# Performance work log

Hardware: AMD Instinct MI355X
Metric: run time of the kernel (lower is better)

Reference implementation:

```python
import jax, jax.numpy as jnp
import numpy as np

L, D, H, M, NC = 12, 768, 12, 3072, 1000
P, IMG, C = 16, 224, 3
HD = D // H // 2  # 32: diff-attn head dim (2*H query heads of HD, H value heads of 2*HD)
B = 32
N = (IMG // P) ** 2 + 1  # 197
EPS = 1e-5


def _layernorm(x, s, b):
    mu = x.mean(-1, keepdims=True)
    var = ((x - mu) ** 2).mean(-1, keepdims=True)
    return (x - mu) * jax.lax.rsqrt(var + EPS) * s + b


def _rmsnorm(x, s):
    ms = (x * x).mean(-1, keepdims=True)
    return x * jax.lax.rsqrt(ms + EPS) * s


def _diff_attn(x, qw, kw, vw, ow, lq1, lk1, lq2, lk2, sls, lam_init):
    b, n, _ = x.shape
    q = (x @ qw).reshape(b, n, 2 * H, HD)
    k = (x @ kw).reshape(b, n, 2 * H, HD)
    v = (x @ vw).reshape(b, n, H, 2 * HD)
    scores = jnp.einsum('bnhd,bmhd->bhnm', q, k) * (HD ** -0.5)
    attn = jax.nn.softmax(scores, axis=-1)  # [b, 2H, n, n]
    lam = jnp.exp(jnp.sum(lq1 * lk1)) - jnp.exp(jnp.sum(lq2 * lk2)) + lam_init
    attn = attn.reshape(b, H, 2, n, n)
    attn = attn[:, :, 0] - lam * attn[:, :, 1]  # differential attention map
    out = jnp.einsum('bhnm,bmhd->bnhd', attn, v)  # [b, n, H, 2*HD]
    out = _rmsnorm(out, sls) * (1.0 - lam_init)
    return out.reshape(b, n, D) @ ow


def _forward(x, conv_w, conv_b, cls_token, pos_emb,
             ln1_s, ln1_b, q_w, k_w, v_w, o_w, lq1, lk1, lq2, lk2, subln_s,
             ln2_s, ln2_b, w1, b1, w2, b2, lnf_s, lnf_b, head_w, head_b):
    # patch embed: conv stride=patch, then flatten to tokens
    h = jax.lax.conv_general_dilated(x, conv_w, (P, P), 'VALID',
                                     dimension_numbers=('NCHW', 'OIHW', 'NCHW'))
    h = h + conv_b[None, :, None, None]
    bsz = x.shape[0]
    h = h.reshape(bsz, D, -1).transpose(0, 2, 1)  # [B, 196, D]
    h = jnp.concatenate([jnp.broadcast_to(cls_token, (bsz, 1, D)), h], axis=1)
    h = h + pos_emb
    for i in range(L):
        lam_init = 0.8 - 0.6 * np.exp(-0.3 * i)
        a = _diff_attn(_layernorm(h, ln1_s[i], ln1_b[i]), q_w[i], k_w[i], v_w[i], o_w[i],
                       lq1[i], lk1[i], lq2[i], lk2[i], subln_s[i], lam_init)
        h = h + a
        m = _layernorm(h, ln2_s[i], ln2_b[i])
        m = jax.nn.gelu(m @ w1[i] + b1[i]) @ w2[i] + b2[i]
        h = h + m
    h = _layernorm(h, lnf_s, lnf_b)
    return h[:, 0] @ head_w + head_b


def setup_inputs() -> dict:
    key = jax.random.key(0)
    ks = iter(jax.random.split(key, 40))
    def rn(shape, s=0.02):
        return jax.random.normal(next(ks), shape, jnp.float32) * s
    return {
        'x': jax.random.normal(next(ks), (B, C, IMG, IMG), jnp.float32),
        'conv_w': rn((D, C, P, P)), 'conv_b': jnp.zeros((D,), jnp.float32),
        'cls_token': jnp.zeros((1, 1, D), jnp.float32),
        'pos_emb': rn((1, N, D)),
        'ln1_s': jnp.ones((L, D), jnp.float32), 'ln1_b': jnp.zeros((L, D), jnp.float32),
        'q_w': rn((L, D, D)), 'k_w': rn((L, D, D)), 'v_w': rn((L, D, D)), 'o_w': rn((L, D, D)),
        'lq1': rn((L, HD), 0.1), 'lk1': rn((L, HD), 0.1),
        'lq2': rn((L, HD), 0.1), 'lk2': rn((L, HD), 0.1),
        'subln_s': jnp.ones((L, 2 * HD), jnp.float32),
        'ln2_s': jnp.ones((L, D), jnp.float32), 'ln2_b': jnp.zeros((L, D), jnp.float32),
        'w1': rn((L, D, M)), 'b1': jnp.zeros((L, M), jnp.float32),
        'w2': rn((L, M, D)), 'b2': jnp.zeros((L, D), jnp.float32),
        'lnf_s': jnp.ones((D,), jnp.float32), 'lnf_b': jnp.zeros((D,), jnp.float32),
        'head_w': rn((D, NC)), 'head_b': jnp.zeros((NC,), jnp.float32),
    }


def reference(x, conv_w, conv_b, cls_token, pos_emb,
              ln1_s, ln1_b, q_w, k_w, v_w, o_w, lq1, lk1, lq2, lk2, subln_s,
              ln2_s, ln2_b, w1, b1, w2, b2, lnf_s, lnf_b, head_w, head_b):
    return _forward(x, conv_w, conv_b, cls_token, pos_emb,
                    ln1_s, ln1_b, q_w, k_w, v_w, o_w, lq1, lk1, lq2, lk2, subln_s,
                    ln2_s, ln2_b, w1, b1, w2, b2, lnf_s, lnf_b, head_w, head_b)
```

## Files before the change

kernel.cpp:

```cpp
#include <hip/hip_runtime.h>
#include <cmath>


typedef unsigned short u16;
typedef u16 u16x4 __attribute__((ext_vector_type(4)));
typedef u16 u16x8 __attribute__((ext_vector_type(8)));
typedef float fx4 __attribute__((ext_vector_type(4)));
typedef __bf16 bf16x8 __attribute__((ext_vector_type(8)));

#define MROWS 6304
#define MPAD  6400

__device__ __forceinline__ float bf2f(u16 u) {
  union { unsigned int i; float f; } c; c.i = ((unsigned int)u) << 16; return c.f;
}
__device__ __forceinline__ u16 f2bf(float f) {
  union { float f; unsigned int i; } c; c.f = f;
  return (u16)((c.i + 0x7FFFu + ((c.i >> 16) & 1u)) >> 16);
}
__device__ __forceinline__ float gelu_f(float x) {
  float u = 0.7978845608028654f * (x + 0.044715f * x * x * x);
  u = fminf(fmaxf(u, -30.f), 30.f);
  float e = __expf(2.f * u);
  return 0.5f * x * (1.f + (e - 1.f) / (e + 1.f));
}

__device__ __forceinline__ void gload16(const void* g, void* l) {
  __builtin_amdgcn_global_load_lds(
      (const __attribute__((address_space(1))) void*)g,
      (__attribute__((address_space(3))) void*)l, 16, 0, 0);
}

__device__ __forceinline__ int xcd_swz(int orig, int nwg) {
  int q = nwg >> 3, r = nwg & 7;
  int x = orig & 7, i = orig >> 3;
  return (x < r ? x * (q + 1) : r * (q + 1) + (x - r) * q) + i;
}

enum { EP_F32 = 0, EP_BF16 = 1, EP_GELU_BF16 = 2, EP_RESID_F32 = 3 };

template<int MODE>
__device__ __forceinline__ void ep_store(void* outp, const float* __restrict__ resid,
                                         size_t m, size_t n, size_t N, float v) {
  if (MODE == EP_GELU_BF16)      ((u16*)outp)[m * N + n] = f2bf(gelu_f(v));
  else if (MODE == EP_BF16)      ((u16*)outp)[m * N + n] = f2bf(v);
  else if (MODE == EP_RESID_F32) ((float*)outp)[m * N + n] = resid[m * N + n] + v;
  else                           ((float*)outp)[m * N + n] = v;
}

template<int MODE, bool BIAS>
__device__ __forceinline__
void gemm_big_body(const u16* __restrict__ A, const u16* __restrict__ Bt,
                   const float* __restrict__ bias, const float* __restrict__ resid,
                   void* __restrict__ outp, int M, int N, int K, int GX)
{
  __shared__ unsigned char lds[2][2 * 128 * 64 * 2];
  const int tid = threadIdx.x;
  const int lane = tid & 63, w = tid >> 6;
  const int g = lane >> 4, l = lane & 15;
  const int wr = w >> 1, wc = w & 1;
  const int wg = xcd_swz(blockIdx.x, gridDim.x);
  const int bm = (wg % GX) * 128, bn = (wg / GX) * 128;

  const int swz_half = ((lane & 7) ^ ((lane >> 3) & 7)) << 3;
  const int srow = 32 * w + (lane >> 3);
  const u16* gA = A + (size_t)(bm + srow) * K + swz_half;
  const u16* gB = Bt + (size_t)(bn + srow) * K + swz_half;

  fx4 acc[4][4] = {};

  auto STAGE = [&](int buf, int kt) {
    unsigned char* bA = &lds[buf][0] + 4096 * w;
    unsigned char* bB = bA + 16384;
    #pragma unroll
    for (int c = 0; c < 4; ++c) {
      gload16(gA + (size_t)(8 * c) * K + kt, bA + (8 * c) * 128);
      gload16(gB + (size_t)(8 * c) * K + kt, bB + (8 * c) * 128);
    }
  };

  STAGE(0, 0);
  __syncthreads();
  int cur = 0;
  for (int kt = 0; kt < K; kt += 64) {
    if (kt + 64 < K) STAGE(cur ^ 1, kt + 64);
    const unsigned char* As = &lds[cur][0];
    const unsigned char* Bs = As + 16384;
    #pragma unroll
    for (int kk = 0; kk < 2; ++kk) {
      bf16x8 af[4], bfr[4];
      #pragma unroll
      for (int i = 0; i < 4; ++i) {
        int ar = wr * 64 + i * 16 + l;
        af[i] = *(const bf16x8*)(As + ar * 128 + ((kk * 64 + g * 16) ^ ((ar & 7) << 4)));
        int br = wc * 64 + i * 16 + l;
        bfr[i] = *(const bf16x8*)(Bs + br * 128 + ((kk * 64 + g * 16) ^ ((br & 7) << 4)));
      }
      #pragma unroll
      for (int i = 0; i < 4; ++i)
        #pragma unroll
        for (int j = 0; j < 4; ++j)
          acc[i][j] = __builtin_amdgcn_mfma_f32_16x16x32_bf16(af[i], bfr[j], acc[i][j], 0, 0, 0);
    }
    __syncthreads();
    cur ^= 1;
  }
  #pragma unroll
  for (int j = 0; j < 4; ++j) {
    int n = bn + wc * 64 + j * 16 + l;
    float bv = BIAS ? bias[n] : 0.f;
    #pragma unroll
    for (int i = 0; i < 4; ++i) {
      int mbase = bm + wr * 64 + i * 16 + g * 4;
      #pragma unroll
      for (int q = 0; q < 4; ++q) {
        int m = mbase + q;
        if (m < M) ep_store<MODE>(outp, resid, m, n, N, acc[i][j][q] + bv);
      }
    }
  }
}

template<int MODE, bool BIAS>
__device__ __forceinline__
void gemm_n64_body(const u16* __restrict__ A, const u16* __restrict__ Bt,
                   const float* __restrict__ bias, const float* __restrict__ resid,
                   void* __restrict__ outp, int M, int N, int K, int NT)
{
  __shared__ unsigned char lds[2][(128 + 64) * 64 * 2];
  const int tid = threadIdx.x;
  const int lane = tid & 63, w = tid >> 6;
  const int g = lane >> 4, l = lane & 15;
  const int wg = xcd_swz(blockIdx.x, gridDim.x);
  const int bm = (wg / NT) * 128, bn = (wg % NT) * 64;

  const int swz_half = ((lane & 7) ^ ((lane >> 3) & 7)) << 3;
  const u16* gA = A + (size_t)(bm + 32 * w + (lane >> 3)) * K + swz_half;
  const u16* gB = Bt + (size_t)(bn + 16 * w + (lane >> 3)) * K + swz_half;

  fx4 acc[2][4] = {};

  auto STAGE = [&](int buf, int kt) {
    unsigned char* bA = &lds[buf][0] + 4096 * w;
    unsigned char* bB = &lds[buf][0] + 16384 + 2048 * w;
    #pragma unroll
    for (int c = 0; c < 4; ++c)
      gload16(gA + (size_t)(8 * c) * K + kt, bA + (8 * c) * 128);
    #pragma unroll
    for (int c = 0; c < 2; ++c)
      gload16(gB + (size_t)(8 * c) * K + kt, bB + (8 * c) * 128);
  };

  STAGE(0, 0);
  __syncthreads();
  int cur = 0;
  for (int kt = 0; kt < K; kt += 64) {
    if (kt + 64 < K) STAGE(cur ^ 1, kt + 64);
    const unsigned char* As = &lds[cur][0];
    const unsigned char* Bs = As + 16384;
    #pragma unroll
    for (int kk = 0; kk < 2; ++kk) {
      bf16x8 af[2], bfr[4];
      #pragma unroll
      for (int i = 0; i < 2; ++i) {
        int ar = w * 32 + i * 16 + l;
        af[i] = *(const bf16x8*)(As + ar * 128 + ((kk * 64 + g * 16) ^ ((ar & 7) << 4)));
      }
      #pragma unroll
      for (int j = 0; j < 4; ++j) {
        int br = j * 16 + l;
        bfr[j] = *(const bf16x8*)(Bs + br * 128 + ((kk * 64 + g * 16) ^ ((br & 7) << 4)));
      }
      #pragma unroll
      for (int i = 0; i < 2; ++i)
        #pragma unroll
        for (int j = 0; j < 4; ++j)
          acc[i][j] = __builtin_amdgcn_mfma_f32_16x16x32_bf16(af[i], bfr[j], acc[i][j], 0, 0, 0);
    }
    __syncthreads();
    cur ^= 1;
  }
  #pragma unroll
  for (int j = 0; j < 4; ++j) {
    int n = bn + j * 16 + l;
    float bv = BIAS ? bias[n] : 0.f;
    #pragma unroll
    for (int i = 0; i < 2; ++i) {
      int mbase = bm + w * 32 + i * 16 + g * 4;
      #pragma unroll
      for (int q = 0; q < 4; ++q) {
        int m = mbase + q;
        if (m < M) ep_store<MODE>(outp, resid, m, n, N, acc[i][j][q] + bv);
      }
    }
  }
}

__global__ __launch_bounds__(256) void patch_gemm(const u16* A, const u16* Bt, float* outp) {
  gemm_n64_body<EP_F32, false>(A, Bt, nullptr, nullptr, outp, 6272, 768, 768, 12);
}
__global__ __launch_bounds__(256) void qkv_gemm(const u16* A, const u16* Bt, u16* outp) {
  gemm_big_body<EP_BF16, false>(A, Bt, nullptr, nullptr, outp, MROWS, 2304, 768, 50);
}
__global__ __launch_bounds__(256) void oproj_gemm(const u16* A, const u16* Bt,
                                                  const float* resid, float* outp) {
  gemm_n64_body<EP_RESID_F32, false>(A, Bt, nullptr, resid, outp, MROWS, 768, 768, 12);
}
__global__ __launch_bounds__(256) void mlp1_gemm(const u16* A, const u16* Bt,
                                                 const float* bias, u16* outp) {
  gemm_big_body<EP_GELU_BF16, true>(A, Bt, bias, nullptr, outp, MROWS, 3072, 768, 50);
}
__global__ __launch_bounds__(256) void mlp2_gemm(const u16* A, const u16* Bt,
                                                 const float* bias, const float* resid,
                                                 float* outp) {
  gemm_n64_body<EP_RESID_F32, true>(A, Bt, bias, resid, outp, MROWS, 768, 3072, 12);
}

template<bool OUTF32>
__global__ __launch_bounds__(64)
void layernorm_k(const float* __restrict__ x, const float* __restrict__ s,
                 const float* __restrict__ b, void* __restrict__ outp, size_t in_rstride)
{
  int r = blockIdx.x, lane = threadIdx.x;
  const fx4* xp = (const fx4*)(x + (size_t)r * in_rstride);
  fx4 v[3];
  float sum = 0.f, sq = 0.f;
  #pragma unroll
  for (int j = 0; j < 3; ++j) {
    v[j] = xp[j * 64 + lane];
    #pragma unroll
    for (int e = 0; e < 4; ++e) { sum += v[j][e]; sq += v[j][e] * v[j][e]; }
  }
  #pragma unroll
  for (int off = 32; off; off >>= 1) { sum += __shfl_xor(sum, off); sq += __shfl_xor(sq, off); }
  float mu = sum * (1.f / 768.f);
  float var = sq * (1.f / 768.f) - mu * mu;
  float rs = rsqrtf(var + 1e-5f);
  const fx4* sp = (const fx4*)s;
  const fx4* bp = (const fx4*)b;
  #pragma unroll
  for (int j = 0; j < 3; ++j) {
    fx4 sv = sp[j * 64 + lane], bv = bp[j * 64 + lane];
    if (OUTF32) {
      fx4 o;
      #pragma unroll
      for (int e = 0; e < 4; ++e) o[e] = (v[j][e] - mu) * rs * sv[e] + bv[e];
      *(fx4*)((float*)outp + (size_t)r * 768 + (j * 64 + lane) * 4) = o;
    } else {
      u16x4 o;
      #pragma unroll
      for (int e = 0; e < 4; ++e) o[e] = f2bf((v[j][e] - mu) * rs * sv[e] + bv[e]);
      *(u16x4*)((u16*)outp + (size_t)r * 768 + (j * 64 + lane) * 4) = o;
    }
  }
}

#define KSTR 40
#define VSTR 232
#define DA_LDS (2 * 224 * KSTR * 2 + 64 * VSTR * 2 + 4 * 16 * VSTR * 2)

__global__ __launch_bounds__(256)
void diff_attn(const u16* __restrict__ qkv, const float* __restrict__ lam_p,
               const float* __restrict__ sls, u16* __restrict__ outp, float lam_init)
{
  extern __shared__ char smem[];
  u16* K1s = (u16*)smem;
  u16* K2s = K1s + 224 * KSTR;
  u16* Vt  = K2s + 224 * KSTR;
  const int tid = threadIdx.x;
  const int w = tid >> 6, lane = tid & 63;
  const int g = lane >> 4, l = lane & 15;
  u16* Pw = Vt + 64 * VSTR + w * 16 * VSTR;

  const int bh = blockIdx.x;
  const int b = bh / 12, hh = bh % 12;
  const u16* base = qkv + (size_t)b * 197 * 2304;

  if (tid < 197) {
    const u16* kr = base + (size_t)tid * 2304 + 768 + hh * 64;
    *(u16x8*)(K1s + tid * KSTR + 0)  = *(const u16x8*)(kr + 0);
    *(u16x8*)(K1s + tid * KSTR + 8)  = *(const u16x8*)(kr + 8);
    *(u16x8*)(K1s + tid * KSTR + 16) = *(const u16x8*)(kr + 16);
    *(u16x8*)(K1s + tid * KSTR + 24) = *(const u16x8*)(kr + 24);
    *(u16x8*)(K2s + tid * KSTR + 0)  = *(const u16x8*)(kr + 32);
    *(u16x8*)(K2s + tid * KSTR + 8)  = *(const u16x8*)(kr + 40);
    *(u16x8*)(K2s + tid * KSTR + 16) = *(const u16x8*)(kr + 48);
    *(u16x8*)(K2s + tid * KSTR + 24) = *(const u16x8*)(kr + 56);
    const u16* vr = base + (size_t)tid * 2304 + 1536 + hh * 64;
    #pragma unroll
    for (int jj = 0; jj < 8; ++jj) {
      u16x8 vv = *(const u16x8*)(vr + jj * 8);
      #pragma unroll
      for (int e = 0; e < 8; ++e) Vt[(jj * 8 + e) * VSTR + tid] = vv[e];
    }
  }
  for (int idx = tid; idx < 64 * 27; idx += 256) {
    Vt[(idx / 27) * VSTR + 197 + (idx % 27)] = 0;
  }
  __syncthreads();

  const float lam = lam_p[0];
  const float oscale = 1.f - lam_init;
  const float scale = 0.17677669529663687f;
  const fx4 zero = {};

  for (int qb = w; qb < 13; qb += 4) {
    const int qbase = qb * 16;
    const u16* qrow = base + (size_t)(qbase + l) * 2304 + hh * 64;
    bf16x8 qf1 = *(const bf16x8*)(qrow + g * 8);
    bf16x8 qf2 = *(const bf16x8*)(qrow + 32 + g * 8);

    fx4 s1[14], s2[14];
    #pragma unroll
    for (int t = 0; t < 14; ++t) {
      bf16x8 kf1 = *(const bf16x8*)(K1s + (t * 16 + l) * KSTR + g * 8);
      bf16x8 kf2 = *(const bf16x8*)(K2s + (t * 16 + l) * KSTR + g * 8);
      s1[t] = __builtin_amdgcn_mfma_f32_16x16x32_bf16(qf1, kf1, zero, 0, 0, 0);
      s2[t] = __builtin_amdgcn_mfma_f32_16x16x32_bf16(qf2, kf2, zero, 0, 0, 0);
    }

    float mx1[4] = {-1e30f, -1e30f, -1e30f, -1e30f};
    float mx2[4] = {-1e30f, -1e30f, -1e30f, -1e30f};
    #pragma unroll
    for (int t = 0; t < 14; ++t) {
      bool ok = (t * 16 + l) < 197;
      #pragma unroll
      for (int q = 0; q < 4; ++q) {
        float v1 = ok ? s1[t][q] * scale : -1e30f;
        float v2 = ok ? s2[t][q] * scale : -1e30f;
        s1[t][q] = v1; s2[t][q] = v2;
        mx1[q] = fmaxf(mx1[q], v1); mx2[q] = fmaxf(mx2[q], v2);
      }
    }
    #pragma unroll
    for (int off = 8; off; off >>= 1)
      #pragma unroll
      for (int q = 0; q < 4; ++q) {
        mx1[q] = fmaxf(mx1[q], __shfl_xor(mx1[q], off));
        mx2[q] = fmaxf(mx2[q], __shfl_xor(mx2[q], off));
      }
    float z1[4] = {0, 0, 0, 0}, z2[4] = {0, 0, 0, 0};
    #pragma unroll
    for (int t = 0; t < 14; ++t)
      #pragma unroll
      for (int q = 0; q < 4; ++q) {
        float p1 = __expf(s1[t][q] - mx1[q]);
        float p2 = __expf(s2[t][q] - mx2[q]);
        s1[t][q] = p1; s2[t][q] = p2;
        z1[q] += p1; z2[q] += p2;
      }
    #pragma unroll
    for (int off = 8; off; off >>= 1)
      #pragma unroll
      for (int q = 0; q < 4; ++q) {
        z1[q] += __shfl_xor(z1[q], off);
        z2[q] += __shfl_xor(z2[q], off);
      }
    float r1[4], r2[4];
    #pragma unroll
    for (int q = 0; q < 4; ++q) { r1[q] = 1.f / z1[q]; r2[q] = lam / z2[q]; }

    #pragma unroll
    for (int t = 0; t < 14; ++t)
      #pragma unroll
      for (int q = 0; q < 4; ++q) {
        float pc = s1[t][q] * r1[q] - s2[t][q] * r2[q];
        Pw[(g * 4 + q) * VSTR + t * 16 + l] = f2bf(pc);
      }

    fx4 o[4] = {};
    #pragma unroll
    for (int mt = 0; mt < 7; ++mt) {
      bf16x8 pa = *(const bf16x8*)(Pw + l * VSTR + mt * 32 + g * 8);
      #pragma unroll
      for (int j = 0; j < 4; ++j) {
        bf16x8 vb = *(const bf16x8*)(Vt + (j * 16 + l) * VSTR + mt * 32 + g * 8);
        o[j] = __builtin_amdgcn_mfma_f32_16x16x32_bf16(pa, vb, o[j], 0, 0, 0);
      }
    }

    float ms[4] = {0, 0, 0, 0};
    #pragma unroll
    for (int j = 0; j < 4; ++j)
      #pragma unroll
      for (int q = 0; q < 4; ++q) ms[q] += o[j][q] * o[j][q];
    #pragma unroll
    for (int off = 8; off; off >>= 1)
      #pragma unroll
      for (int q = 0; q < 4; ++q) ms[q] += __shfl_xor(ms[q], off);
    float rr[4];
    #pragma unroll
    for (int q = 0; q < 4; ++q) rr[q] = rsqrtf(ms[q] * (1.f / 64.f) + 1e-5f) * oscale;
    #pragma unroll
    for (int j = 0; j < 4; ++j) {
      float slv = sls[j * 16 + l];
      #pragma unroll
      for (int q = 0; q < 4; ++q) {
        int row = qbase + g * 4 + q;
        if (row < 197)
          outp[(size_t)(b * 197 + row) * 768 + hh * 64 + j * 16 + l] = f2bf(o[j][q] * rr[q] * slv);
      }
    }
  }
}

__global__ __launch_bounds__(256)
void prep_weights(const float* __restrict__ qw, const float* __restrict__ kw,
                  const float* __restrict__ vw, const float* __restrict__ ow,
                  const float* __restrict__ w1, const float* __restrict__ w2,
                  u16* __restrict__ qkvt, u16* __restrict__ ot,
                  u16* __restrict__ w1t, u16* __restrict__ w2t,
                  const float* __restrict__ lq1, const float* __restrict__ lk1,
                  const float* __restrict__ lq2, const float* __restrict__ lk2,
                  float* __restrict__ lam_out, float lam_init)
{
  int bid = blockIdx.x;
  if (bid == 1728) {
    if (threadIdx.x < 64) {
      int lane = threadIdx.x;
      float p1 = lane < 32 ? lq1[lane] * lk1[lane] : 0.f;
      float p2 = lane < 32 ? lq2[lane] * lk2[lane] : 0.f;
      #pragma unroll
      for (int off = 32; off; off >>= 1) { p1 += __shfl_xor(p1, off); p2 += __shfl_xor(p2, off); }
      if (lane == 0) lam_out[0] = __expf(p1) - __expf(p2) + lam_init;
    }
    return;
  }
  const float* src; u16* dst; int Kd, Nd, tx, ty;
  if (bid < 576) {
    int which = bid / 144, t = bid % 144;
    ty = t / 12; tx = t % 12; Kd = 768; Nd = 768;
    src = (which == 0) ? qw : (which == 1) ? kw : (which == 2) ? vw : ow;
    dst = (which < 3) ? (qkvt + (size_t)which * 768 * 768) : ot;
  } else if (bid < 1152) {
    int t = bid - 576; ty = t / 12; tx = t % 12; Kd = 768; Nd = 3072; src = w1; dst = w1t;
  } else {
    int t = bid - 1152; ty = t / 48; tx = t % 48; Kd = 3072; Nd = 768; src = w2; dst = w2t;
  }
  __shared__ u16 tile[64][65];
  int tid2 = threadIdx.x;
  int k0 = tx * 64, n0 = ty * 64;
  #pragma unroll
  for (int j = 0; j < 16; ++j) {
    int idx = j * 256 + tid2;
    int rr = idx >> 6, cc = idx & 63;
    tile[rr][cc] = f2bf(src[(size_t)(k0 + rr) * Nd + n0 + cc]);
  }
  __syncthreads();
  #pragma unroll
  for (int j = 0; j < 16; ++j) {
    int idx = j * 256 + tid2;
    int rr = idx >> 6, cc = idx & 63;
    dst[(size_t)(n0 + rr) * Kd + k0 + cc] = tile[cc][rr];
  }
}

__global__ void convert_cw(const float* __restrict__ src, u16* __restrict__ dst)
{
  int i4 = blockIdx.x * 256 + threadIdx.x;
  fx4 v = *(const fx4*)(src + (size_t)i4 * 4);
  u16x4 o;
  #pragma unroll
  for (int e = 0; e < 4; ++e) o[e] = f2bf(v[e]);
  *(u16x4*)(dst + (size_t)i4 * 4) = o;
}

__global__ void im2col(const float* __restrict__ x, u16* __restrict__ A0)
{
  int i4 = blockIdx.x * 256 + threadIdx.x;
  int base = i4 * 4;
  int r = base / 768, c0 = base % 768;
  int b = r / 196, p = r % 196;
  int py = p / 14, px = p % 14;
  int ch = c0 >> 8;
  int cc = c0 & 255;
  int iy = cc >> 4, ix = cc & 15;
  const float* src = x + (((size_t)(b * 3 + ch) * 224 + py * 16 + iy) * 224 + px * 16 + ix);
  fx4 v = *(const fx4*)src;
  u16x4 o;
  #pragma unroll
  for (int e = 0; e < 4; ++e) o[e] = f2bf(v[e]);
  *(u16x4*)(A0 + base) = o;
}

__global__ void assemble(const float* __restrict__ tmp, const float* __restrict__ conv_b,
                         const float* __restrict__ cls, const float* __restrict__ pos,
                         float* __restrict__ h)
{
  int i4 = blockIdx.x * 256 + threadIdx.x;
  int base = i4 * 4;
  int r = base / 768, d = base % 768;
  int b = r / 197, n = r % 197;
  fx4 pv = *(const fx4*)(pos + (size_t)n * 768 + d);
  fx4 v;
  if (n == 0) {
    v = *(const fx4*)(cls + d);
  } else {
    v = *(const fx4*)(tmp + (size_t)(b * 196 + n - 1) * 768 + d);
    fx4 cb = *(const fx4*)(conv_b + d);
    v = v + cb;
  }
  *(fx4*)(h + (size_t)r * 768 + d) = v + pv;
}

__global__ __launch_bounds__(256)
void head_kernel(const float* __restrict__ ln, const float* __restrict__ hw,
                 const float* __restrict__ hb, float* __restrict__ outp)
{
  int r = blockIdx.x;
  int c = blockIdx.y * 256 + threadIdx.x;
  if (c >= 1000) return;
  const float* lr = ln + (size_t)r * 768;
  float acc = hb[c];
  for (int d = 0; d < 768; ++d)
    acc = fmaf(lr[d], hw[(size_t)d * 1000 + c], acc);
  outp[r * 1000 + c] = acc;
}

extern "C" void kernel_launch(void* const* d_in, const int* in_sizes, int n_in,
                              void* d_out, int out_size, void* d_ws, size_t ws_size,
                              hipStream_t stream)
{
  (void)in_sizes; (void)n_in; (void)out_size; (void)ws_size;
  const float* x      = (const float*)d_in[0];
  const float* conv_w = (const float*)d_in[1];
  const float* conv_b = (const float*)d_in[2];
  const float* cls    = (const float*)d_in[3];
  const float* pos    = (const float*)d_in[4];
  const float* ln1_s  = (const float*)d_in[5];
  const float* ln1_b  = (const float*)d_in[6];
  const float* q_w    = (const float*)d_in[7];
  const float* k_w    = (const float*)d_in[8];
  const float* v_w    = (const float*)d_in[9];
  const float* o_w    = (const float*)d_in[10];
  const float* lq1    = (const float*)d_in[11];
  const float* lk1    = (const float*)d_in[12];
  const float* lq2    = (const float*)d_in[13];
  const float* lk2    = (const float*)d_in[14];
  const float* slsx   = (const float*)d_in[15];
  const float* ln2_s  = (const float*)d_in[16];
  const float* ln2_b  = (const float*)d_in[17];
  const float* w1     = (const float*)d_in[18];
  const float* b1     = (const float*)d_in[19];
  const float* w2     = (const float*)d_in[20];
  const float* b2     = (const float*)d_in[21];
  const float* lnf_s  = (const float*)d_in[22];
  const float* lnf_b  = (const float*)d_in[23];
  const float* head_w = (const float*)d_in[24];
  const float* head_b = (const float*)d_in[25];
  float* out = (float*)d_out;

  char* ws = (char*)d_ws;
  size_t off = 0;
  auto alloc = [&](size_t bytes) { size_t p = off; off += (bytes + 255) & ~(size_t)255; return p; };
  u16*   A_bf  = (u16*)  (ws + alloc((size_t)MPAD * 768 * 2));
  u16*   big   = (u16*)  (ws + alloc((size_t)MPAD * 3072 * 2));
  float* h     = (float*)(ws + alloc((size_t)MROWS * 768 * 4));
  u16*   wqkv  = (u16*)  (ws + alloc((size_t)2304 * 768 * 2));
  u16*   wo    = (u16*)  (ws + alloc((size_t)768 * 768 * 2));
  u16*   w1t   = (u16*)  (ws + alloc((size_t)3072 * 768 * 2));
  u16*   w2t   = (u16*)  (ws + alloc((size_t)768 * 3072 * 2));
  float* lnf_o = (float*)(ws + alloc((size_t)32 * 768 * 4));
  float* lam   = (float*)(ws + alloc(256));
  float* convtmp = (float*)big;
  u16*   cwbf  = w1t;

  hipFuncSetAttribute((const void*)diff_attn,
                      hipFuncAttributeMaxDynamicSharedMemorySize, DA_LDS);

  convert_cw<<<576, 256, 0, stream>>>(conv_w, cwbf);
  im2col<<<4704, 256, 0, stream>>>(x, A_bf);
  patch_gemm<<<588, 256, 0, stream>>>(A_bf, cwbf, convtmp);
  assemble<<<4728, 256, 0, stream>>>(convtmp, conv_b, cls, pos, h);

  for (int l = 0; l < 12; ++l) {
    float lam_init = 0.8f - 0.6f * expf(-0.3f * (float)l);
    prep_weights<<<1729, 256, 0, stream>>>(
        q_w + (size_t)l * 589824, k_w + (size_t)l * 589824,
        v_w + (size_t)l * 589824, o_w + (size_t)l * 589824,
        w1 + (size_t)l * 2359296, w2 + (size_t)l * 2359296,
        wqkv, wo, w1t, w2t,
        lq1 + l * 32, lk1 + l * 32, lq2 + l * 32, lk2 + l * 32,
        lam, lam_init);
    layernorm_k<false><<<MROWS, 64, 0, stream>>>(h, ln1_s + l * 768, ln1_b + l * 768, A_bf, (size_t)768);
    qkv_gemm<<<900, 256, 0, stream>>>(A_bf, wqkv, big);
    diff_attn<<<384, 256, DA_LDS, stream>>>(big, lam, slsx + l * 64, A_bf, lam_init);
    oproj_gemm<<<600, 256, 0, stream>>>(A_bf, wo, h, h);
    layernorm_k<false><<<MROWS, 64, 0, stream>>>(h, ln2_s + l * 768, ln2_b + l * 768, A_bf, (size_t)768);
    mlp1_gemm<<<1200, 256, 0, stream>>>(A_bf, w1t, b1 + l * 3072, big);
    mlp2_gemm<<<600, 256, 0, stream>>>(big, w2t, b2 + l * 768, h, h);
  }

  layernorm_k<true><<<32, 64, 0, stream>>>(h, lnf_s, lnf_b, lnf_o, (size_t)197 * 768);
  head_kernel<<<dim3(32, 4), 256, 0, stream>>>(lnf_o, head_w, head_b, out);
}
```

Before: 3.205 ms.

## Overlap next-tile global loads with MFMA via explicit vmcnt waits; N-major tile order

Replaces the full __syncthreads drain in both GEMM bodies with explicit s_waitcnt vmcnt waits that only wait for the current tile's async LDS loads, so the prefetch of the next K-tile can remain in flight during the MFMA loop. Sched barriers keep the compiler from moving LDS reads across the barriers. The big GEMM also changes block-to-tile mapping so consecutive workgroups walk along N for the same M rows, which is meant to improve A-tile reuse in cache. Hand-counted vmcnt values risk races if the number of outstanding loads differs from what the counts assume.

```diff
diff --git a/kernel.cpp b/kernel.cpp
--- a/kernel.cpp
+++ b/kernel.cpp
@@ -10,6 +10,8 @@
 
 #define MROWS 6304
 #define MPAD  6400
+
+#define WAITV(N) asm volatile("s_waitcnt vmcnt(" #N ")" ::: "memory")
 
 __device__ __forceinline__ float bf2f(u16 u) {
   union { unsigned int i; float f; } c; c.i = ((unsigned int)u) << 16; return c.f;
@@ -52,7 +54,7 @@
 __device__ __forceinline__
 void gemm_big_body(const u16* __restrict__ A, const u16* __restrict__ Bt,
                    const float* __restrict__ bias, const float* __restrict__ resid,
-                   void* __restrict__ outp, int M, int N, int K, int GX)
+                   void* __restrict__ outp, int M, int N, int K, int NT)
 {
   __shared__ unsigned char lds[2][2 * 128 * 64 * 2];
   const int tid = threadIdx.x;
@@ -60,7 +62,7 @@
   const int g = lane >> 4, l = lane & 15;
   const int wr = w >> 1, wc = w & 1;
   const int wg = xcd_swz(blockIdx.x, gridDim.x);
-  const int bm = (wg % GX) * 128, bn = (wg / GX) * 128;
+  const int bm = (wg / NT) * 128, bn = (wg % NT) * 128;
 
   const int swz_half = ((lane & 7) ^ ((lane >> 3) & 7)) << 3;
   const int srow = 32 * w + (lane >> 3);
@@ -80,10 +82,16 @@
   };
 
   STAGE(0, 0);
-  __syncthreads();
   int cur = 0;
   for (int kt = 0; kt < K; kt += 64) {
-    if (kt + 64 < K) STAGE(cur ^ 1, kt + 64);
+    if (kt + 64 < K) {
+      STAGE(cur ^ 1, kt + 64);
+      WAITV(8);
+    } else {
+      WAITV(0);
+    }
+    __builtin_amdgcn_s_barrier();
+    __builtin_amdgcn_sched_barrier(0);
     const unsigned char* As = &lds[cur][0];
     const unsigned char* Bs = As + 16384;
     #pragma unroll
@@ -102,7 +110,8 @@
         for (int j = 0; j < 4; ++j)
           acc[i][j] = __builtin_amdgcn_mfma_f32_16x16x32_bf16(af[i], bfr[j], acc[i][j], 0, 0, 0);
     }
-    __syncthreads();
+    __builtin_amdgcn_sched_barrier(0);
+    __builtin_amdgcn_s_barrier();
     cur ^= 1;
   }
   #pragma unroll
@@ -152,10 +161,16 @@
   };
 
   STAGE(0, 0);
-  __syncthreads();
   int cur = 0;
   for (int kt = 0; kt < K; kt += 64) {
-    if (kt + 64 < K) STAGE(cur ^ 1, kt + 64);
+    if (kt + 64 < K) {
+      STAGE(cur ^ 1, kt + 64);
+      WAITV(6);
+    } else {
+      WAITV(0);
+    }
+    __builtin_amdgcn_s_barrier();
+    __builtin_amdgcn_sched_barrier(0);
     const unsigned char* As = &lds[cur][0];
     const unsigned char* Bs = As + 16384;
     #pragma unroll
@@ -177,7 +192,8 @@
         for (int j = 0; j < 4; ++j)
           acc[i][j] = __builtin_amdgcn_mfma_f32_16x16x32_bf16(af[i], bfr[j], acc[i][j], 0, 0, 0);
     }
-    __syncthreads();
+    __builtin_amdgcn_sched_barrier(0);
+    __builtin_amdgcn_s_barrier();
     cur ^= 1;
   }
   #pragma unroll
@@ -200,7 +216,7 @@
   gemm_n64_body<EP_F32, false>(A, Bt, nullptr, nullptr, outp, 6272, 768, 768, 12);
 }
 __global__ __launch_bounds__(256) void qkv_gemm(const u16* A, const u16* Bt, u16* outp) {
-  gemm_big_body<EP_BF16, false>(A, Bt, nullptr, nullptr, outp, MROWS, 2304, 768, 50);
+  gemm_big_body<EP_BF16, false>(A, Bt, nullptr, nullptr, outp, MROWS, 2304, 768, 18);
 }
 __global__ __launch_bounds__(256) void oproj_gemm(const u16* A, const u16* Bt,
                                                   const float* resid, float* outp) {
@@ -208,7 +224,7 @@
 }
 __global__ __launch_bounds__(256) void mlp1_gemm(const u16* A, const u16* Bt,
                                                  const float* bias, u16* outp) {
-  gemm_big_body<EP_GELU_BF16, true>(A, Bt, bias, nullptr, outp, MROWS, 3072, 768, 50);
+  gemm_big_body<EP_GELU_BF16, true>(A, Bt, bias, nullptr, outp, MROWS, 3072, 768, 24);
 }
 __global__ __launch_bounds__(256) void mlp2_gemm(const u16* A, const u16* Bt,
                                                  const float* bias, const float* resid,
```

Measured after the change: 3.118 ms. 2.7% less time.
